# Performance work log

Hardware: AMD Instinct MI355X
Metric: run time of the kernel (lower is better)

## Reference

```python
import jax, jax.numpy as jnp
import numpy as np

SIZE_IN = 8192
SIZE_OUT = 8192


def setup_inputs() -> dict:
    key = jax.random.key(0)
    ks = jax.random.split(key, 10)
    fan_in = SIZE_IN
    bound = 1.0 / np.sqrt(fan_in)
    x = jax.random.normal(ks[0], (SIZE_IN,), dtype=jnp.float32)
    saturated = jax.random.randint(ks[1], (SIZE_IN,), 0, 2).astype(jnp.bool_)
    # dense linear params (kaiming-uniform-ish)
    weight = jax.random.uniform(ks[2], (SIZE_OUT, SIZE_IN), jnp.float32, -bound, bound)
    bias = jax.random.uniform(ks[3], (SIZE_OUT,), jnp.float32, -bound, bound)
    # per-neuron bud MLPs: Linear(3,3) -> relu -> Linear(3,3) -> relu -> Linear(3,size_out) -> relu
    b3_bound = 1.0 / np.sqrt(3.0)
    W1 = jax.random.uniform(ks[4], (SIZE_IN, 3, 3), jnp.float32, -b3_bound, b3_bound)
    b1 = jax.random.uniform(ks[5], (SIZE_IN, 3), jnp.float32, -b3_bound, b3_bound)
    W2 = jax.random.uniform(ks[6], (SIZE_IN, 3, 3), jnp.float32, -b3_bound, b3_bound)
    b2 = jax.random.uniform(ks[7], (SIZE_IN, 3), jnp.float32, -b3_bound, b3_bound)
    W3 = jax.random.uniform(ks[8], (SIZE_IN, SIZE_OUT, 3), jnp.float32, -b3_bound, b3_bound)
    b3 = jax.random.uniform(ks[9], (SIZE_IN, SIZE_OUT), jnp.float32, -b3_bound, b3_bound)
    return {"x": x, "saturated": saturated, "weight": weight, "bias": bias,
            "W1": W1, "b1": b1, "W2": W2, "b2": b2, "W3": W3, "b3": b3}


def reference(x, saturated, weight, bias, W1, b1, W2, b2, W3, b3):
    sat_f = saturated.astype(x.dtype)
    x_b = x * sat_f
    mask = (x_b != 0).astype(x.dtype)  # buds exist for nonzero saturated neurons
    h0 = jnp.broadcast_to((x * (1.0 / 3.0))[:, None], (x.shape[0], 3))  # [N,3]
    # torch Linear: y = h @ W^T + b, W is [out,in]
    h1 = jax.nn.relu(jnp.einsum('ni,noi->no', h0, W1) + b1)  # [N,3]
    h2 = jax.nn.relu(jnp.einsum('ni,noi->no', h1, W2) + b2)  # [N,3]
    h3 = jax.nn.relu(jnp.einsum('ni,noi->no', h2, W3) + b3)  # [N,size_out]
    u = jnp.sum(h3 * mask[:, None], axis=0)  # sum over active buds -> [size_out]
    x_masked = x * (1.0 - sat_f)  # zero saturated neurons before dense linear
    out = weight @ x_masked + bias + u
    return out
```

## Files before the change

### kernel.cpp

```cpp
#include <hip/hip_runtime.h>

#define N_IN 8192
#define N_OUT 8192

__global__ __launch_bounds__(256) void k1_prep(
    const float* __restrict__ x, const int* __restrict__ sat,
    const float* __restrict__ W1, const float* __restrict__ b1,
    const float* __restrict__ W2, const float* __restrict__ b2,
    float4* __restrict__ h2buf, float* __restrict__ xmbuf)
{
    int k = blockIdx.x * blockDim.x + threadIdx.x;
    if (k >= N_IN) return;
    float xs = x[k];
    bool s = (sat[k] != 0);
    xmbuf[k] = s ? 0.0f : xs;

    const float* w1 = W1 + (size_t)k * 9;
    const float* B1 = b1 + (size_t)k * 3;
    float x3 = xs * (1.0f / 3.0f);
    float h1[3];
#pragma unroll
    for (int i = 0; i < 3; ++i) {
        float v = x3 * (w1[3*i] + w1[3*i+1] + w1[3*i+2]) + B1[i];
        h1[i] = v > 0.0f ? v : 0.0f;
    }
    const float* w2 = W2 + (size_t)k * 9;
    const float* B2 = b2 + (size_t)k * 3;
    float h2[3];
#pragma unroll
    for (int i = 0; i < 3; ++i) {
        float v = w2[3*i] * h1[0] + w2[3*i+1] * h1[1] + w2[3*i+2] * h1[2] + B2[i];
        h2[i] = v > 0.0f ? v : 0.0f;
    }
    float flag = (s && xs != 0.0f) ? 1.0f : 0.0f;
    h2buf[k] = make_float4(h2[0], h2[1], h2[2], flag);
}

__global__ __launch_bounds__(256) void k2_dense(
    const float* __restrict__ weight, const float* __restrict__ bias,
    const float* __restrict__ xm, float* __restrict__ out)
{
    int wave = threadIdx.x >> 6;
    int lane = threadIdx.x & 63;
    int o = blockIdx.x * 4 + wave;

    const float4* wrow = (const float4*)(weight + (size_t)o * N_IN);
    const float4* xv   = (const float4*)xm;

    float sum = 0.0f;
#pragma unroll 4
    for (int it = 0; it < N_IN / 4 / 64; ++it) {
        int idx = it * 64 + lane;
        float4 w = wrow[idx];
        float4 v = xv[idx];
        sum += w.x * v.x + w.y * v.y + w.z * v.z + w.w * v.w;
    }
#pragma unroll
    for (int off = 32; off; off >>= 1) sum += __shfl_down(sum, off);
    if (lane == 0) out[o] = bias[o] + sum;
}

__global__ __launch_bounds__(256) void k3_bud(
    const float* __restrict__ W3, const float* __restrict__ b3,
    const float4* __restrict__ h2buf, float* __restrict__ out)
{
    int otile  = blockIdx.x & 7;
    int kchunk = blockIdx.x >> 3;
    int o  = otile * 1024 + threadIdx.x * 4;
    int k0 = kchunk * 64;

    float acc0 = 0.0f, acc1 = 0.0f, acc2 = 0.0f, acc3 = 0.0f;

    for (int kk = 0; kk < 64; ++kk) {
        int k = k0 + kk;
        float4 h = h2buf[k];
        if (h.w == 0.0f) continue;

        const float4* wp = (const float4*)(W3 + ((size_t)k * N_OUT + o) * 3);
        float4 a = wp[0], b = wp[1], c = wp[2];
        float4 bb = *(const float4*)(b3 + (size_t)k * N_OUT + o);

        float t0 = h.x * a.x + h.y * a.y + h.z * a.z + bb.x;
        float t1 = h.x * a.w + h.y * b.x + h.z * b.y + bb.y;
        float t2 = h.x * b.z + h.y * b.w + h.z * c.x + bb.z;
        float t3 = h.x * c.y + h.y * c.z + h.z * c.w + bb.w;
        acc0 += t0 > 0.0f ? t0 : 0.0f;
        acc1 += t1 > 0.0f ? t1 : 0.0f;
        acc2 += t2 > 0.0f ? t2 : 0.0f;
        acc3 += t3 > 0.0f ? t3 : 0.0f;
    }

    unsafeAtomicAdd(out + o + 0, acc0);
    unsafeAtomicAdd(out + o + 1, acc1);
    unsafeAtomicAdd(out + o + 2, acc2);
    unsafeAtomicAdd(out + o + 3, acc3);
}

extern "C" void kernel_launch(void* const* d_in, const int* in_sizes, int n_in,
                              void* d_out, int out_size, void* d_ws, size_t ws_size,
                              hipStream_t stream)
{
    const float* x    = (const float*)d_in[0];
    const int*   sat  = (const int*)  d_in[1];
    const float* wgt  = (const float*)d_in[2];
    const float* bias = (const float*)d_in[3];
    const float* W1   = (const float*)d_in[4];
    const float* b1   = (const float*)d_in[5];
    const float* W2   = (const float*)d_in[6];
    const float* b2   = (const float*)d_in[7];
    const float* W3   = (const float*)d_in[8];
    const float* b3   = (const float*)d_in[9];
    float* out = (float*)d_out;

    float4* h2buf = (float4*)d_ws;
    float*  xmbuf = (float*)((char*)d_ws + N_IN * sizeof(float4));

    k1_prep<<<N_IN / 256, 256, 0, stream>>>(x, sat, W1, b1, W2, b2, h2buf, xmbuf);
    k2_dense<<<N_OUT / 4, 256, 0, stream>>>(wgt, bias, xmbuf, out);
    k3_bud<<<1024, 256, 0, stream>>>(W3, b3, h2buf, out);
}
```

Before: 1.202 ms.

## Fuse prep into dense and bud kernels, compact active buds, use nontemporal loads

Removes the separate prep kernel. The dense kernel now applies the saturation mask inline, and the bud kernel computes the small per-neuron MLP into shared memory for its 64-neuron chunk. A ballot builds a compacted list of active buds so the main loop only iterates over active k, and large weight streams use nontemporal loads. The aim is to save a launch and the workspace round trip and to cut branch divergence. In exchange, the MLP is recomputed redundantly in each of the 8 output tiles per chunk, and dense reads the sat array alongside x.

```diff
diff --git a/kernel.cpp b/kernel.cpp
--- a/kernel.cpp
+++ b/kernel.cpp
@@ -3,82 +3,105 @@
 #define N_IN 8192
 #define N_OUT 8192
 
-__global__ __launch_bounds__(256) void k1_prep(
+typedef float f4 __attribute__((ext_vector_type(4)));
+typedef int   i4 __attribute__((ext_vector_type(4)));
+
+__global__ __launch_bounds__(256) void kd_dense(
+    const float* __restrict__ weight, const float* __restrict__ bias,
     const float* __restrict__ x, const int* __restrict__ sat,
-    const float* __restrict__ W1, const float* __restrict__ b1,
-    const float* __restrict__ W2, const float* __restrict__ b2,
-    float4* __restrict__ h2buf, float* __restrict__ xmbuf)
-{
-    int k = blockIdx.x * blockDim.x + threadIdx.x;
-    if (k >= N_IN) return;
-    float xs = x[k];
-    bool s = (sat[k] != 0);
-    xmbuf[k] = s ? 0.0f : xs;
-
-    const float* w1 = W1 + (size_t)k * 9;
-    const float* B1 = b1 + (size_t)k * 3;
-    float x3 = xs * (1.0f / 3.0f);
-    float h1[3];
-#pragma unroll
-    for (int i = 0; i < 3; ++i) {
-        float v = x3 * (w1[3*i] + w1[3*i+1] + w1[3*i+2]) + B1[i];
-        h1[i] = v > 0.0f ? v : 0.0f;
-    }
-    const float* w2 = W2 + (size_t)k * 9;
-    const float* B2 = b2 + (size_t)k * 3;
-    float h2[3];
-#pragma unroll
-    for (int i = 0; i < 3; ++i) {
-        float v = w2[3*i] * h1[0] + w2[3*i+1] * h1[1] + w2[3*i+2] * h1[2] + B2[i];
-        h2[i] = v > 0.0f ? v : 0.0f;
-    }
-    float flag = (s && xs != 0.0f) ? 1.0f : 0.0f;
-    h2buf[k] = make_float4(h2[0], h2[1], h2[2], flag);
-}
-
-__global__ __launch_bounds__(256) void k2_dense(
-    const float* __restrict__ weight, const float* __restrict__ bias,
-    const float* __restrict__ xm, float* __restrict__ out)
+    float* __restrict__ out)
 {
     int wave = threadIdx.x >> 6;
     int lane = threadIdx.x & 63;
     int o = blockIdx.x * 4 + wave;
 
-    const float4* wrow = (const float4*)(weight + (size_t)o * N_IN);
-    const float4* xv   = (const float4*)xm;
+    const f4* wrow = (const f4*)(weight + (size_t)o * N_IN);
+    const f4* xv   = (const f4*)x;
+    const i4* sv   = (const i4*)sat;
 
     float sum = 0.0f;
-#pragma unroll 4
+#pragma unroll 8
     for (int it = 0; it < N_IN / 4 / 64; ++it) {
         int idx = it * 64 + lane;
-        float4 w = wrow[idx];
-        float4 v = xv[idx];
-        sum += w.x * v.x + w.y * v.y + w.z * v.z + w.w * v.w;
+        f4 w = __builtin_nontemporal_load(wrow + idx);
+        f4 v = xv[idx];
+        i4 s = sv[idx];
+        float vx = s.x ? 0.0f : v.x;
+        float vy = s.y ? 0.0f : v.y;
+        float vz = s.z ? 0.0f : v.z;
+        float vw = s.w ? 0.0f : v.w;
+        sum += w.x * vx + w.y * vy + w.z * vz + w.w * vw;
     }
 #pragma unroll
     for (int off = 32; off; off >>= 1) sum += __shfl_down(sum, off);
     if (lane == 0) out[o] = bias[o] + sum;
 }
 
-__global__ __launch_bounds__(256) void k3_bud(
+__global__ __launch_bounds__(256) void kb_bud(
+    const float* __restrict__ x, const int* __restrict__ sat,
+    const float* __restrict__ W1, const float* __restrict__ b1,
+    const float* __restrict__ W2, const float* __restrict__ b2,
     const float* __restrict__ W3, const float* __restrict__ b3,
-    const float4* __restrict__ h2buf, float* __restrict__ out)
+    float* __restrict__ out)
 {
+    __shared__ f4  sh2[64];
+    __shared__ int slist[64];
+    __shared__ int snact;
+
     int otile  = blockIdx.x & 7;
     int kchunk = blockIdx.x >> 3;
-    int o  = otile * 1024 + threadIdx.x * 4;
-    int k0 = kchunk * 64;
+    int k0  = kchunk * 64;
+    int tid = threadIdx.x;
 
+    if (tid < 64) {
+        int k = k0 + tid;
+        float xs = x[k];
+        bool s = (sat[k] != 0);
+
+        const float* w1 = W1 + (size_t)k * 9;
+        const float* B1 = b1 + (size_t)k * 3;
+        float x3 = xs * (1.0f / 3.0f);
+        float h1[3];
+#pragma unroll
+        for (int i = 0; i < 3; ++i) {
+            float v = x3 * (w1[3*i] + w1[3*i+1] + w1[3*i+2]) + B1[i];
+            h1[i] = v > 0.0f ? v : 0.0f;
+        }
+        const float* w2 = W2 + (size_t)k * 9;
+        const float* B2 = b2 + (size_t)k * 3;
+        float h2[3];
+#pragma unroll
+        for (int i = 0; i < 3; ++i) {
+            float v = w2[3*i] * h1[0] + w2[3*i+1] * h1[1] + w2[3*i+2] * h1[2] + B2[i];
+            h2[i] = v > 0.0f ? v : 0.0f;
+        }
+
+        bool act = s && (xs != 0.0f);
+        unsigned long long m = __ballot(act);
+        if (act) {
+            int pos = __popcll(m & ((1ull << tid) - 1ull));
+            slist[pos] = tid;
+        }
+        if (tid == 0) snact = __popcll(m);
+        f4 hv; hv.x = h2[0]; hv.y = h2[1]; hv.z = h2[2]; hv.w = 0.0f;
+        sh2[tid] = hv;
+    }
+    __syncthreads();
+
+    int nact = snact;
+    int o = otile * 1024 + tid * 4;
     float acc0 = 0.0f, acc1 = 0.0f, acc2 = 0.0f, acc3 = 0.0f;
 
-    for (int kk = 0; kk < 64; ++kk) {
-        int k = k0 + kk;
-        float4 h = h2buf[k];
-        if (h.w == 0.0f) continue;
-
-        const float4* wp = (const float4*)(W3 + ((size_t)k * N_OUT + o) * 3);
-        float4 a = wp[0], b = wp[1], c = wp[2];
-        float4 bb = *(const float4*)(b3 + (size_t)k * N_OUT + o);
+#pragma unroll 4
+    for (int j = 0; j < nact; ++j) {
+        int kk = slist[j];
+        f4 h = sh2[kk];
+        size_t base = (size_t)(k0 + kk) * N_OUT + o;
+        const f4* wp = (const f4*)(W3 + base * 3);
+        f4 a  = __builtin_nontemporal_load(wp);
+        f4 b  = __builtin_nontemporal_load(wp + 1);
+        f4 c  = __builtin_nontemporal_load(wp + 2);
+        f4 bb = __builtin_nontemporal_load((const f4*)(b3 + base));
 
         float t0 = h.x * a.x + h.y * a.y + h.z * a.z + bb.x;
         float t1 = h.x * a.w + h.y * b.x + h.z * b.y + bb.y;
@@ -112,10 +135,6 @@
     const float* b3   = (const float*)d_in[9];
     float* out = (float*)d_out;
 
-    float4* h2buf = (float4*)d_ws;
-    float*  xmbuf = (float*)((char*)d_ws + N_IN * sizeof(float4));
-
-    k1_prep<<<N_IN / 256, 256, 0, stream>>>(x, sat, W1, b1, W2, b2, h2buf, xmbuf);
-    k2_dense<<<N_OUT / 4, 256, 0, stream>>>(wgt, bias, xmbuf, out);
-    k3_bud<<<1024, 256, 0, stream>>>(W3, b3, h2buf, out);
+    kd_dense<<<N_OUT / 4, 256, 0, stream>>>(wgt, bias, x, sat, out);
+    kb_bud<<<1024, 256, 0, stream>>>(x, sat, W1, b1, W2, b2, W3, b3, out);
 }
```

Result: slower. 1.268 ms (+5.5%).
